# Kernel tuning notes

Hardware: AMD Instinct MI355X
Metric: run time of the kernel (lower is better)

## Reference

```python
import jax, jax.numpy as jnp
import numpy as np

B, C, H, W = 16, 192, 96, 96
L = 60  # number of stanh quantization levels (codebook size)


def setup_inputs() -> dict:
    key = jax.random.key(0)
    k1, k2, k3 = jax.random.split(key, 3)
    # latent y (pre-quantization) -- scaled so it spans the codebook range
    inputs = jax.random.normal(k1, (B, C, H, W), dtype=jnp.float32) * 5.0
    means = jax.random.normal(k2, (B, C, H, W), dtype=jnp.float32)
    # sorted unique quantization levels (stanh.unique_values); strictly increasing
    base = jnp.linspace(-15.0, 15.0, L, dtype=jnp.float32)
    jitter = jax.random.normal(k3, (L,), dtype=jnp.float32) * 0.05
    codebook = jnp.sort(base + jitter).astype(jnp.float32)
    return {"inputs": inputs, "means": means, "codebook": codebook}


def reference(inputs, means, codebook):
    """quantize(mode='symbols') + dequantize of GaussianConditionalStanh.

    Original: per-element Python loop calling transform_map, i.e.
    argmin_l |codebook[l] - (x - mean)| -> int symbol; dequantize gathers
    codebook[symbol] and adds the mean back (removing_mean=True).
    Vectorized here as a searchsorted over codebook midpoints (exact
    nearest neighbor for a sorted 1-D codebook).
    """
    y = inputs - means                              # [B,C,H,W]
    mid = 0.5 * (codebook[:-1] + codebook[1:])      # [L-1] decision boundaries
    idx = jnp.searchsorted(mid, y)                  # nearest-level index in [0, L)
    symbols = idx.astype(jnp.int32)                 # integer symbols
    dequant = jnp.take(codebook, idx) + means       # map_cdf_sos gather + means
    return symbols, dequant
```

## Files before the change

kernel.cpp:

```cpp
#include <hip/hip_runtime.h>
#include <math.h>


namespace {

constexpr int kL = 60;

__device__ __forceinline__ int find_idx(float y, const float* __restrict__ ms,
                                        float c0, float invd) {
    float t = (y - c0) * invd + 0.5f;
    int g = (int)t;
    g = max(0, min(g, kL - 1));
    while (y > ms[g + 1]) ++g;
    while (y <= ms[g]) --g;
    return g;
}

__global__ __launch_bounds__(256) void stanh_quant_kernel(
    const float* __restrict__ x,
    const float* __restrict__ mean,
    const float* __restrict__ cb,
    float* __restrict__ sym_out,
    float* __restrict__ deq_out,
    int n4)
{
    __shared__ float cb_s[kL];
    __shared__ float ms[kL + 4];

    const int tid = threadIdx.x;
    if (tid < kL) cb_s[tid] = cb[tid];
    if (tid == 0) ms[0] = -INFINITY;
    if (tid < kL - 1) ms[tid + 1] = 0.5f * (cb[tid] + cb[tid + 1]);
    if (tid >= kL - 1 && tid < kL + 3) ms[tid + 1] = INFINITY;
    __syncthreads();

    const float c0 = cb[0];
    const float invd = 59.0f / (cb[kL - 1] - c0);

    const float4* __restrict__ x4 = (const float4*)x;
    const float4* __restrict__ m4 = (const float4*)mean;
    float4* __restrict__ s4 = (float4*)sym_out;
    float4* __restrict__ d4 = (float4*)deq_out;

    const int stride = gridDim.x * blockDim.x;
    for (int g = blockIdx.x * blockDim.x + tid; g < n4; g += stride) {
        const float4 xv = x4[g];
        const float4 mv = m4[g];
        const float y0 = xv.x - mv.x;
        const float y1 = xv.y - mv.y;
        const float y2 = xv.z - mv.z;
        const float y3 = xv.w - mv.w;

        const int i0 = find_idx(y0, ms, c0, invd);
        const int i1 = find_idx(y1, ms, c0, invd);
        const int i2 = find_idx(y2, ms, c0, invd);
        const int i3 = find_idx(y3, ms, c0, invd);

        float4 sv;
        sv.x = (float)i0; sv.y = (float)i1; sv.z = (float)i2; sv.w = (float)i3;
        float4 dv;
        dv.x = cb_s[i0] + mv.x;
        dv.y = cb_s[i1] + mv.y;
        dv.z = cb_s[i2] + mv.z;
        dv.w = cb_s[i3] + mv.w;

        s4[g] = sv;
        d4[g] = dv;
    }
}

}

extern "C" void kernel_launch(void* const* d_in, const int* in_sizes, int n_in,
                              void* d_out, int out_size, void* d_ws, size_t ws_size,
                              hipStream_t stream) {
    const float* x    = (const float*)d_in[0];
    const float* mean = (const float*)d_in[1];
    const float* cb   = (const float*)d_in[2];

    const int n = in_sizes[0];
    float* sym_out = (float*)d_out;
    float* deq_out = sym_out + n;

    const int n4 = n / 4;
    const int block = 256;
    int grid = 8192;
    const int max_grid = (n4 + block - 1) / block;
    if (grid > max_grid) grid = max_grid;

    hipLaunchKernelGGL(stanh_quant_kernel, dim3(grid), dim3(block), 0, stream,
                       x, mean, cb, sym_out, deq_out, n4);
}
```

Before: 369.9 us.

## Use fixed-work blocks with batched nontemporal vector loads and stores

Replaces the grid-stride loop with one-shot blocks, each handling four float4 chunks per thread. All loads for a thread are issued up front as nontemporal vector loads, and the outputs are written with nontemporal stores. This is meant to raise memory-level parallelism and avoid cache pollution in a bandwidth-bound streaming kernel. The cost is a larger grid, so each block re-runs the shared-memory codebook setup, and register pressure goes up.

```diff
diff --git a/kernel.cpp b/kernel.cpp
--- a/kernel.cpp
+++ b/kernel.cpp
@@ -5,6 +5,7 @@
 namespace {
 
 constexpr int kL = 60;
+typedef float f4 __attribute__((ext_vector_type(4)));
 
 __device__ __forceinline__ int find_idx(float y, const float* __restrict__ ms,
                                         float c0, float invd) {
@@ -37,35 +38,65 @@
     const float c0 = cb[0];
     const float invd = 59.0f / (cb[kL - 1] - c0);
 
-    const float4* __restrict__ x4 = (const float4*)x;
-    const float4* __restrict__ m4 = (const float4*)mean;
-    float4* __restrict__ s4 = (float4*)sym_out;
-    float4* __restrict__ d4 = (float4*)deq_out;
+    const f4* __restrict__ x4 = (const f4*)x;
+    const f4* __restrict__ m4 = (const f4*)mean;
+    f4* __restrict__ s4 = (f4*)sym_out;
+    f4* __restrict__ d4 = (f4*)deq_out;
 
-    const int stride = gridDim.x * blockDim.x;
-    for (int g = blockIdx.x * blockDim.x + tid; g < n4; g += stride) {
-        const float4 xv = x4[g];
-        const float4 mv = m4[g];
-        const float y0 = xv.x - mv.x;
-        const float y1 = xv.y - mv.y;
-        const float y2 = xv.z - mv.z;
-        const float y3 = xv.w - mv.w;
+    const int base = blockIdx.x * 1024 + tid;
 
-        const int i0 = find_idx(y0, ms, c0, invd);
-        const int i1 = find_idx(y1, ms, c0, invd);
-        const int i2 = find_idx(y2, ms, c0, invd);
-        const int i3 = find_idx(y3, ms, c0, invd);
+    if (base + 3 * 256 < n4) {
+        f4 xv[4], mv[4];
+#pragma unroll
+        for (int i = 0; i < 4; ++i) {
+            xv[i] = __builtin_nontemporal_load(x4 + base + i * 256);
+            mv[i] = __builtin_nontemporal_load(m4 + base + i * 256);
+        }
 
-        float4 sv;
-        sv.x = (float)i0; sv.y = (float)i1; sv.z = (float)i2; sv.w = (float)i3;
-        float4 dv;
-        dv.x = cb_s[i0] + mv.x;
-        dv.y = cb_s[i1] + mv.y;
-        dv.z = cb_s[i2] + mv.z;
-        dv.w = cb_s[i3] + mv.w;
+        int idx[4][4];
+#pragma unroll
+        for (int i = 0; i < 4; ++i) {
+            idx[i][0] = find_idx(xv[i].x - mv[i].x, ms, c0, invd);
+            idx[i][1] = find_idx(xv[i].y - mv[i].y, ms, c0, invd);
+            idx[i][2] = find_idx(xv[i].z - mv[i].z, ms, c0, invd);
+            idx[i][3] = find_idx(xv[i].w - mv[i].w, ms, c0, invd);
+        }
 
-        s4[g] = sv;
-        d4[g] = dv;
+#pragma unroll
+        for (int i = 0; i < 4; ++i) {
+            f4 sv;
+            sv.x = (float)idx[i][0];
+            sv.y = (float)idx[i][1];
+            sv.z = (float)idx[i][2];
+            sv.w = (float)idx[i][3];
+            f4 dv;
+            dv.x = cb_s[idx[i][0]] + mv[i].x;
+            dv.y = cb_s[idx[i][1]] + mv[i].y;
+            dv.z = cb_s[idx[i][2]] + mv[i].z;
+            dv.w = cb_s[idx[i][3]] + mv[i].w;
+            __builtin_nontemporal_store(sv, s4 + base + i * 256);
+            __builtin_nontemporal_store(dv, d4 + base + i * 256);
+        }
+    } else {
+        for (int i = 0; i < 4; ++i) {
+            const int g = base + i * 256;
+            if (g >= n4) break;
+            const f4 xv = x4[g];
+            const f4 mv = m4[g];
+            const int i0 = find_idx(xv.x - mv.x, ms, c0, invd);
+            const int i1 = find_idx(xv.y - mv.y, ms, c0, invd);
+            const int i2 = find_idx(xv.z - mv.z, ms, c0, invd);
+            const int i3 = find_idx(xv.w - mv.w, ms, c0, invd);
+            f4 sv;
+            sv.x = (float)i0; sv.y = (float)i1; sv.z = (float)i2; sv.w = (float)i3;
+            f4 dv;
+            dv.x = cb_s[i0] + mv.x;
+            dv.y = cb_s[i1] + mv.y;
+            dv.z = cb_s[i2] + mv.z;
+            dv.w = cb_s[i3] + mv.w;
+            s4[g] = sv;
+            d4[g] = dv;
+        }
     }
 }
 
@@ -84,9 +115,8 @@
 
     const int n4 = n / 4;
     const int block = 256;
-    int grid = 8192;
-    const int max_grid = (n4 + block - 1) / block;
-    if (grid > max_grid) grid = max_grid;
+    const int per_block = block * 4;
+    const int grid = (n4 + per_block - 1) / per_block;
 
     hipLaunchKernelGGL(stanh_quant_kernel, dim3(grid), dim3(block), 0, stream,
                        x, mean, cb, sym_out, deq_out, n4);
```

Result: faster. 357.9 us (-3.2%).
